# Optimization experiments

Hardware: AMD Instinct MI355X
Metric: run time of the kernel (lower is better)

The kernel has to match this reference:

```python
import jax, jax.numpy as jnp
import numpy as np

ND, NPR, DD, DP, LAT, AT, B = 2048, 2048, 128, 128, 128, 32, 16384


def setup_inputs():
    key = jax.random.key(0)
    ks = jax.random.split(key, 20)
    s = 0.05
    d = {}
    d["e_p_adj"] = (jax.random.uniform(ks[0], (ND, NPR)) < 0.05).astype(jnp.float32)
    d["e_e_adj"] = (jax.random.uniform(ks[1], (ND, ND)) < 0.05).astype(jnp.float32)
    d["p_p_adj"] = (jax.random.uniform(ks[2], (NPR, NPR)) < 0.05).astype(jnp.float32)
    d["input_disease"] = jax.random.randint(ks[3], (B,), 0, ND)
    d["input_drug"] = jax.random.randint(ks[4], (B,), 0, NPR)
    d["labels"] = jax.random.randint(ks[5], (B,), 0, 2)
    # learned parameters
    d["disease_emb"] = jax.random.normal(ks[6], (ND, DD)) * s
    d["drug_emb"] = jax.random.normal(ks[7], (NPR, DP)) * s
    d["Wdg"] = jax.random.normal(ks[8], (DP, LAT)) * s   # disease_gcn_w
    d["bdg_lin"] = jnp.zeros((LAT,))                      # Linear bias
    d["bdg"] = jnp.zeros((LAT,))                          # extra disease_gcn_b
    d["Wpg"] = jax.random.normal(ks[9], (DD, LAT)) * s   # drug_gcn_w
    d["bpg_lin"] = jnp.zeros((LAT,))
    d["bpg"] = jnp.zeros((LAT,))
    d["Wa1_d"] = jax.random.normal(ks[10], (DP + DD, AT)) * s  # concat [key(drug), query(disease)]
    d["ba1_d"] = jnp.zeros((AT,))
    d["Wa2_d"] = jax.random.normal(ks[11], (AT, 1)) * s
    d["ba2_d"] = jnp.zeros((1,))
    d["Wa1_p"] = jax.random.normal(ks[12], (DD + DP, AT)) * s  # concat [key(disease), query(drug)]
    d["ba1_p"] = jnp.zeros((AT,))
    d["Wa2_p"] = jax.random.normal(ks[13], (AT, 1)) * s
    d["ba2_p"] = jnp.zeros((1,))
    d["Wd2"] = jax.random.normal(ks[14], (DD, LAT)) * s  # disease_w2
    d["bd2"] = jnp.zeros((LAT,))
    d["Wp3"] = jax.random.normal(ks[15], (DP, LAT)) * s  # drug_w3
    d["bp3"] = jnp.zeros((LAT,))
    d["mlp_W1"] = jax.random.normal(ks[16], (LAT, DD)) * s
    d["mlp_b1"] = jnp.zeros((DD,))
    d["mlp_W2"] = jax.random.normal(ks[17], (DD, DD)) * s
    d["mlp_b2"] = jnp.zeros((DD,))
    d["Wpred"] = jax.random.normal(ks[18], (DD, 1)) * s
    d["bpred"] = jnp.zeros((1,))
    return d


def _attention_gcn(adj, other, selfe, W1, b1, W2, b2):
    # torch: concat([key=other, query=self]) -> Linear(W1) ; split W1 instead of
    # materializing the [Ns, No, Dk+Dq] concat tensor (same math, less HBM traffic)
    do = other.shape[1]
    ko = other @ W1[:do]              # [No, A]
    qs = selfe @ W1[do:]              # [Ns, A]
    h = jax.nn.relu(qs[:, None, :] + ko[None, :, :] + b1)   # [Ns, No, A]
    alpha = jax.nn.relu(jnp.squeeze(h @ W2, -1) + b2[0])    # [Ns, No]
    alpha = alpha * adj
    return jax.nn.softmax(alpha, axis=1) @ other            # [Ns, Do]


def _forward(e_p_adj, e_e_adj, p_p_adj, input_disease, input_drug, labels,
             disease_emb, drug_emb, Wdg, bdg_lin, bdg, Wpg, bpg_lin, bpg,
             Wa1_d, ba1_d, Wa2_d, ba2_d, Wa1_p, ba1_p, Wa2_p, ba2_p,
             Wd2, bd2, Wp3, bp3, mlp_W1, mlp_b1, mlp_W2, mlp_b2, Wpred, bpred):
    h_e_gcn = _attention_gcn(e_p_adj, drug_emb, disease_emb, Wa1_d, ba1_d, Wa2_d, ba2_d)
    h_e_gcn = h_e_gcn @ Wdg + bdg_lin + bdg
    h_p_gcn = _attention_gcn(e_p_adj.T, disease_emb, drug_emb, Wa1_p, ba1_p, Wa2_p, ba2_p)
    h_p_gcn = h_p_gcn @ Wpg + bpg_lin + bpg
    # disease knn branch
    deg_d = jnp.sum(e_e_adj, axis=1, keepdims=True) + 1e-8
    h_e_e = ((e_e_adj @ disease_emb) / deg_d) @ Wd2 + bd2
    h_e = jax.nn.selu(h_e_gcn + h_e_e)
    # drug knn branch
    deg_p = jnp.sum(p_p_adj, axis=1, keepdims=True) + 1e-8
    h_p_p = ((p_p_adj @ drug_emb) / deg_p) @ Wp3 + bp3
    h_p = jax.nn.selu(h_p_gcn + h_p_p)
    # pair prediction MLP
    x = h_e[input_disease] * h_p[input_drug]                # [B, LAT]
    x = jax.nn.selu(x @ mlp_W1 + mlp_b1)
    x = jax.nn.selu(x @ mlp_W2 + mlp_b2)
    z = jnp.squeeze(x @ Wpred, -1) + bpred[0]               # [B]
    y = labels.astype(jnp.float32)
    # BCEWithLogitsLoss (stable), mean reduction
    loss = jnp.mean(jnp.maximum(z, 0.0) - z * y + jnp.log1p(jnp.exp(-jnp.abs(z))))
    return (loss, jax.nn.sigmoid(z))


def reference(e_p_adj, e_e_adj, p_p_adj, input_disease, input_drug, labels,
              disease_emb, drug_emb, Wdg, bdg_lin, bdg, Wpg, bpg_lin, bpg,
              Wa1_d, ba1_d, Wa2_d, ba2_d, Wa1_p, ba1_p, Wa2_p, ba2_p,
              Wd2, bd2, Wp3, bp3, mlp_W1, mlp_b1, mlp_W2, mlp_b2, Wpred, bpred):
    return _forward(e_p_adj, e_e_adj, p_p_adj, input_disease, input_drug, labels,
                    disease_emb, drug_emb, Wdg, bdg_lin, bdg, Wpg, bpg_lin, bpg,
                    Wa1_d, ba1_d, Wa2_d, ba2_d, Wa1_p, ba1_p, Wa2_p, ba2_p,
                    Wd2, bd2, Wp3, bp3, mlp_W1, mlp_b1, mlp_W2, mlp_b2, Wpred, bpred)
```

## Files before the change

kernel.cpp:

```cpp
#include <hip/hip_runtime.h>

#define ND   2048
#define BB   16384

typedef unsigned short u16;
typedef unsigned int u32;
typedef __attribute__((ext_vector_type(8))) short short8;
typedef __attribute__((ext_vector_type(4))) float f32x4;

__device__ inline float bf2f(u16 u) {
    union { u32 i; float f; } v; v.i = ((u32)u) << 16; return v.f;
}
__device__ inline u16 f2bf(float f) {
    union { float f; u32 i; } v; v.f = f;
    u32 i = v.i + 0x7fffu + ((v.i >> 16) & 1u);
    return (u16)(i >> 16);
}
__device__ inline float seluf(float x) {
    const float sc = 1.0507009873554805f, al = 1.6732632423543772f;
    return x > 0.f ? sc * x : sc * al * expm1f(x);
}
__device__ inline short8 packbf8(float4 f0, float4 f1) {
    short8 a;
    a[0] = (short)f2bf(f0.x); a[1] = (short)f2bf(f0.y);
    a[2] = (short)f2bf(f0.z); a[3] = (short)f2bf(f0.w);
    a[4] = (short)f2bf(f1.x); a[5] = (short)f2bf(f1.y);
    a[6] = (short)f2bf(f1.z); a[7] = (short)f2bf(f1.w);
    return a;
}

__global__ void detectk(const void* __restrict__ demb, u32* __restrict__ flag) {
    const u16* p = (const u16*)demb;
    int tid = threadIdx.x;
    int sane = 0;
    #pragma unroll
    for (int i = 0; i < 2; i++) {
        u16 u = p[4 * tid + 2 * i];
        int e = (u >> 7) & 0xFF;
        if (u == 0 || (e >= 0x66 && e <= 0x8C)) sane++;
    }
    __shared__ int red[256];
    red[tid] = sane; __syncthreads();
    for (int o = 128; o > 0; o >>= 1) {
        if (tid < o) red[tid] += red[tid + o];
        __syncthreads();
    }
    if (tid == 0) flag[0] = (red[0] < 300) ? 1u : 0u;
}

#define NSEG 26
struct CvtArgs { const void* src[NSEG]; int off[NSEG]; int n[NSEG]; };

__global__ __launch_bounds__(256) void cvtk(CvtArgs a, u16* __restrict__ base,
                                            const u32* __restrict__ flag) {
    int seg = blockIdx.y;
    int n = a.n[seg];
    const void* s = a.src[seg];
    u16* d = base + a.off[seg];
    bool f32 = flag[0] != 0;
    int stride = gridDim.x * blockDim.x;
    for (int i = blockIdx.x * blockDim.x + threadIdx.x; i < n; i += stride)
        d[i] = f32 ? f2bf(((const float*)s)[i]) : ((const u16*)s)[i];
}

__device__ inline void tpose_body(const u16* in, int R, int C,
                                  u16* out, int ldo, int ooff,
                                  u16 (*tile)[33]) {
    int c0 = blockIdx.x * 32, r0 = blockIdx.y * 32;
    int x = c0 + threadIdx.x;
    for (int i = threadIdx.y; i < 32; i += 8) {
        int r = r0 + i;
        tile[i][threadIdx.x] = (r < R && x < C) ? in[(size_t)r * C + x] : (u16)0;
    }
    __syncthreads();
    int rr = r0 + threadIdx.x;
    for (int i = threadIdx.y; i < 32; i += 8) {
        int cc = c0 + i;
        if (cc < C && rr < R) out[(size_t)cc * ldo + ooff + rr] = tile[threadIdx.x][i];
    }
}

__global__ void tpose_smalls(const u16* s0, const u16* s1, const u16* s2,
                             const u16* s3, const u16* s4, const u16* s5,
                             u16* W1T, u16* W2T, u16* WcTe, u16* WcTp) {
    __shared__ u16 tile[32][33];
    const u16* in; u16* out; int ldo, ooff;
    switch (blockIdx.z) {
        case 0:  in = s0; out = W1T;  ldo = 128; ooff = 0;   break;
        case 1:  in = s1; out = W2T;  ldo = 128; ooff = 0;   break;
        case 2:  in = s2; out = WcTe; ldo = 256; ooff = 0;   break;
        case 3:  in = s3; out = WcTe; ldo = 256; ooff = 128; break;
        case 4:  in = s4; out = WcTp; ldo = 256; ooff = 0;   break;
        default: in = s5; out = WcTp; ldo = 256; ooff = 128; break;
    }
    tpose_body(in, 128, 128, out, ldo, ooff, tile);
}

__global__ __launch_bounds__(256) void colsump(const u16* __restrict__ demb,
                                               const u16* __restrict__ pemb,
                                               float* __restrict__ part) {
    int m = blockIdx.y;
    const u16* e = m ? pemb : demb;
    int t = threadIdx.x;
    int c2 = t & 63, rg = t >> 6;
    int r0 = blockIdx.x * 64;
    float s0 = 0.f, s1 = 0.f;
    for (int i = 0; i < 16; i++) {
        u32 v = *(const u32*)(e + (size_t)(r0 + i * 4 + rg) * 128 + c2 * 2);
        s0 += bf2f((u16)(v & 0xffffu));
        s1 += bf2f((u16)(v >> 16));
    }
    __shared__ float t0[256], t1[256];
    t0[t] = s0; t1[t] = s1;
    __syncthreads();
    if (t < 64) {
        float a0 = t0[t] + t0[t + 64] + t0[t + 128] + t0[t + 192];
        float a1 = t1[t] + t1[t + 64] + t1[t + 128] + t1[t + 192];
        part[(size_t)m * 4096 + blockIdx.x * 128 + t * 2 + 0] = a0;
        part[(size_t)m * 4096 + blockIdx.x * 128 + t * 2 + 1] = a1;
    }
}

__global__ void biasc(const u16* a0, const u16* a1, const u16* a2, u16* o0,
                      const u16* b0, const u16* b1, const u16* b2, u16* o1,
                      const float* __restrict__ part,
                      float* __restrict__ csd, float* __restrict__ csp) {
    int t = threadIdx.x;
    o0[t] = f2bf(bf2f(a0[t]) + bf2f(a1[t]) + bf2f(a2[t]));
    o1[t] = f2bf(bf2f(b0[t]) + bf2f(b1[t]) + bf2f(b2[t]));
    float sd = 0.f, sp = 0.f;
    for (int b = 0; b < 32; b++) {
        sd += part[b * 128 + t];
        sp += part[4096 + b * 128 + t];
    }
    csd[t] = sd;
    csp[t] = sp;
}

__global__ __launch_bounds__(128) void koqs(
    const u16* __restrict__ demb, const u16* __restrict__ pemb,
    const u16* __restrict__ Wa1d, const u16* __restrict__ ba1d,
    const u16* __restrict__ Wa1p, const u16* __restrict__ ba1p,
    float* __restrict__ ko_d, float* __restrict__ qs_d,
    float* __restrict__ ko_p, float* __restrict__ qs_p) {
    int row = blockIdx.x, m = blockIdx.y, tid = threadIdx.x;
    const u16* src; const u16* W; const u16* bias; float* out;
    switch (m) {
        case 0:  src = pemb; W = Wa1d;            bias = nullptr; out = ko_d; break;
        case 1:  src = demb; W = Wa1d + 128 * 32; bias = ba1d;    out = qs_d; break;
        case 2:  src = demb; W = Wa1p;            bias = nullptr; out = ko_p; break;
        default: src = pemb; W = Wa1p + 128 * 32; bias = ba1p;    out = qs_p; break;
    }
    __shared__ float x[128];
    __shared__ float red[128];
    x[tid] = bf2f(src[(size_t)row * 128 + tid]);
    __syncthreads();
    int a = tid & 31, part = tid >> 5;
    float s = 0.f;
    #pragma unroll
    for (int k = 0; k < 32; k++) s += x[part * 32 + k] * bf2f(W[(part * 32 + k) * 32 + a]);
    red[tid] = s;
    __syncthreads();
    if (part == 0) {
        float t = red[a] + red[a + 32] + red[a + 64] + red[a + 96];
        if (bias) t += bf2f(bias[a]);
        out[(size_t)row * 32 + a] = t;
    }
}

struct CS {
    const void* adj[3];
    u16* ridx[3]; u32* rcnt[3];
    u16* cidx; u32* ccnt;
};

__global__ __launch_bounds__(256) void csrbuild(CS c, const u32* __restrict__ flag) {
    int m = blockIdx.y, r = blockIdx.x, t = threadIdx.x;
    int lane = t & 63;
    bool f32 = flag[0] != 0;
    __shared__ u32 lcnt;
    if (t == 0) lcnt = 0;
    __syncthreads();
    float v[8];
    int c0 = t * 8;
    if (f32) {
        const float4* p = (const float4*)((const float*)c.adj[m] + (size_t)r * 2048 + c0);
        float4 x = p[0], y = p[1];
        v[0] = x.x; v[1] = x.y; v[2] = x.z; v[3] = x.w;
        v[4] = y.x; v[5] = y.y; v[6] = y.z; v[7] = y.w;
    } else {
        const uint4* p = (const uint4*)((const u16*)c.adj[m] + (size_t)r * 2048 + c0);
        uint4 x = p[0];
        u32 u[4] = {x.x, x.y, x.z, x.w};
        #pragma unroll
        for (int i = 0; i < 4; i++) {
            v[2 * i + 0] = (u[i] & 0xffffu) ? 1.f : 0.f;
            v[2 * i + 1] = (u[i] >> 16)     ? 1.f : 0.f;
        }
    }
    int cnt = 0;
    #pragma unroll
    for (int i = 0; i < 8; i++) cnt += (v[i] != 0.f) ? 1 : 0;
    int pfx = cnt;
    #pragma unroll
    for (int o = 1; o < 64; o <<= 1) {
        int s = __shfl_up(pfx, o, 64);
        if (lane >= o) pfx += s;
    }
    int wtot = __shfl(pfx, 63, 64);
    u32 wb = 0;
    if (lane == 0) wb = atomicAdd(&lcnt, (u32)wtot);
    wb = __shfl((int)wb, 0, 64);
    int o = (int)wb + pfx - cnt;
    u16* ridx = c.ridx[m] + (size_t)r * 2048;
    #pragma unroll
    for (int i = 0; i < 8; i++) {
        if (v[i] != 0.f) {
            ridx[o++] = (u16)(c0 + i);
            if (m == 0) {
                u32 q = atomicAdd(&c.ccnt[c0 + i], 1u);
                c.cidx[(size_t)(c0 + i) * 2048 + q] = (u16)r;
            }
        }
    }
    __syncthreads();
    if (t == 0) c.rcnt[m][r] = lcnt;
}

struct SP {
    const u16* idx[4]; const u32* cnt[4];
    const float* ko[4]; const float* qs[4];
    const u16* w2[4]; const u16* b2[4];
    const u16* emb[4]; const float* csum[4];
    u16* out[4]; int ooff[4]; int attn[4];
};

__global__ __launch_bounds__(256) void spagg(SP a) {
    int task = blockIdx.y;
    int tid = threadIdx.x;
    int wv = tid >> 6, lane = tid & 63;
    int grp = lane >> 4, dim = lane & 15;
    int r = blockIdx.x * 4 + wv;
    const u16* idx = a.idx[task] + (size_t)r * 2048;
    int nnz = (int)a.cnt[task][r];
    int isat = a.attn[task];
    const u16* emb = a.emb[task];
    const float* ko = a.ko[task];

    float qsr[32], w2h[32];
    float b2v = 0.f;
    if (isat) {
        const float4* qp = (const float4*)(a.qs[task] + (size_t)r * 32);
        #pragma unroll
        for (int i = 0; i < 8; i++) {
            float4 v = qp[i];
            qsr[4 * i + 0] = v.x; qsr[4 * i + 1] = v.y;
            qsr[4 * i + 2] = v.z; qsr[4 * i + 3] = v.w;
        }
        #pragma unroll
        for (int i = 0; i < 32; i++) w2h[i] = bf2f(a.w2[task][i]);
        b2v = bf2f(a.b2[task][0]);
    }

    float acc[8];
    #pragma unroll
    for (int t = 0; t < 8; t++) acc[t] = 0.f;
    float wsuml = 0.f;

    for (int base = 0; base < nnz; base += 64) {
        int i = base + lane;
        float w = 0.f;
        int j = 0;
        if (i < nnz) {
            j = (int)idx[i];
            if (isat) {
                const float4* kp = (const float4*)(ko + (size_t)j * 32);
                float s = 0.f;
                #pragma unroll
                for (int q = 0; q < 8; q++) {
                    float4 kv = kp[q];
                    s += fmaxf(qsr[4 * q + 0] + kv.x, 0.f) * w2h[4 * q + 0];
                    s += fmaxf(qsr[4 * q + 1] + kv.y, 0.f) * w2h[4 * q + 1];
                    s += fmaxf(qsr[4 * q + 2] + kv.z, 0.f) * w2h[4 * q + 2];
                    s += fmaxf(qsr[4 * q + 3] + kv.w, 0.f) * w2h[4 * q + 3];
                }
                w = __expf(fmaxf(s + b2v, 0.f)) - 1.f;
            } else {
                w = 1.f;
            }
        }
        wsuml += w;
        int cend = min(64, nnz - base);
        #pragma unroll 4
        for (int k4 = 0; k4 < cend; k4 += 4) {
            int kk = k4 + grp;
            float wk = __shfl(w, kk, 64);
            int jk = __shfl(j, kk, 64);
            const uint4* p = (const uint4*)((const char*)emb + jk * 256 + dim * 16);
            uint4 vv = *p;
            u32 u[4] = {vv.x, vv.y, vv.z, vv.w};
            #pragma unroll
            for (int cc = 0; cc < 4; cc++) {
                acc[2 * cc + 0] = fmaf(wk, bf2f((u16)(u[cc] & 0xffffu)), acc[2 * cc + 0]);
                acc[2 * cc + 1] = fmaf(wk, bf2f((u16)(u[cc] >> 16)), acc[2 * cc + 1]);
            }
        }
    }

    #pragma unroll
    for (int t = 0; t < 8; t++) {
        acc[t] += __shfl_xor(acc[t], 32, 64);
        acc[t] += __shfl_xor(acc[t], 16, 64);
    }
    #pragma unroll
    for (int o = 32; o > 0; o >>= 1) wsuml += __shfl_xor(wsuml, o, 64);

    if (grp == 0) {
        float v[8];
        if (isat) {
            float sc = 1.f / (2048.f + wsuml);
            const float* cs = a.csum[task] + dim * 8;
            #pragma unroll
            for (int t = 0; t < 8; t++) v[t] = (cs[t] + acc[t]) * sc;
        } else {
            float sc = 1.f / (wsuml + 1e-8f);
            #pragma unroll
            for (int t = 0; t < 8; t++) v[t] = acc[t] * sc;
        }
        uint4 pk;
        pk.x = (u32)f2bf(v[0]) | ((u32)f2bf(v[1]) << 16);
        pk.y = (u32)f2bf(v[2]) | ((u32)f2bf(v[3]) << 16);
        pk.z = (u32)f2bf(v[4]) | ((u32)f2bf(v[5]) << 16);
        pk.w = (u32)f2bf(v[6]) | ((u32)f2bf(v[7]) << 16);
        *(uint4*)(a.out[task] + (size_t)r * 256 + a.ooff[task] + dim * 8) = pk;
    }
}

struct GD4 {
    const void* A[4]; const u16* BT[4]; u16* C[4];
    const u16* bias[4]; const float* rs[4];
    int lda[4], ldb[4], ldc[4], coff[4], kiters[4], act[4], araw[4], rsmode[4];
};

#define PADK 136

__global__ __launch_bounds__(256, 2) void gemmL(GD4 g, const u32* __restrict__ flag) {
    __shared__ __align__(16) u16 As[16][PADK];
    __shared__ __align__(16) u16 Bs[128][PADK];
    int z = blockIdx.y;
    bool af32 = g.araw[z] && (flag[0] != 0);
    const void* A = g.A[z];
    const u16* BT = g.BT[z];
    int lda = g.lda[z], ldb = g.ldb[z];
    int kiters = g.kiters[z];
    int tid = threadIdx.x;
    int lane = tid & 63, wv = tid >> 6;
    int mrow = lane & 15, quad = lane >> 4;
    int m0 = blockIdx.x * 16;
    int c0 = wv * 32;
    int sr = tid >> 4, sk = (tid & 15) * 8;
    f32x4 acc0 = {0.f, 0.f, 0.f, 0.f}, acc1 = {0.f, 0.f, 0.f, 0.f};

    short8 ra, rb[8];
    auto ldstage = [&](int kb) {
        if (af32) {
            const float* A32 = (const float*)A;
            const float4* p = (const float4*)(A32 + (size_t)(m0 + sr) * lda + kb + sk);
            float4 f0 = p[0], f1 = p[1];
            ra = packbf8(f0, f1);
        } else {
            ra = *(const short8*)((const u16*)A + (size_t)(m0 + sr) * lda + kb + sk);
        }
        const u16* bbase = BT + (size_t)sr * ldb + kb + sk;
        #pragma unroll
        for (int i = 0; i < 8; i++)
            rb[i] = *(const short8*)(bbase + (size_t)i * 16 * ldb);
    };
    auto ststage = [&]() {
        *(short8*)(&As[sr][sk]) = ra;
        #pragma unroll
        for (int i = 0; i < 8; i++)
            *(short8*)(&Bs[i * 16 + sr][sk]) = rb[i];
    };
    auto compute = [&]() {
        #pragma unroll
        for (int ks = 0; ks < 4; ks++) {
            short8 af = *(const short8*)(&As[mrow][ks * 32 + quad * 8]);
            short8 b0 = *(const short8*)(&Bs[c0 + mrow][ks * 32 + quad * 8]);
            short8 b1 = *(const short8*)(&Bs[c0 + 16 + mrow][ks * 32 + quad * 8]);
            acc0 = __builtin_amdgcn_mfma_f32_16x16x32_bf16(af, b0, acc0, 0, 0, 0);
            acc1 = __builtin_amdgcn_mfma_f32_16x16x32_bf16(af, b1, acc1, 0, 0, 0);
        }
    };

    ldstage(0);
    #pragma unroll 1
    for (int it = 0; it < kiters - 1; ++it) {
        ststage();
        __syncthreads();
        ldstage((it + 1) * 128);
        compute();
        __syncthreads();
    }
    ststage();
    __syncthreads();
    compute();

    const float* rs = g.rs[z];
    int rsmode = g.rsmode[z];
    const u16* bi = g.bias[z];
    u16* C = g.C[z];
    int ldc = g.ldc[z], coff = g.coff[z], act = g.act[z];
    int n0 = c0 + mrow, n1 = n0 + 16;
    float bv0 = bi ? bf2f(bi[n0]) : 0.f;
    float bv1 = bi ? bf2f(bi[n1]) : 0.f;
    #pragma unroll
    for (int r = 0; r < 4; r++) {
        int row = m0 + quad * 4 + r;
        float v0 = acc0[r], v1 = acc1[r];
        if (rsmode == 1) { float sc = rs[row]; v0 *= sc; v1 *= sc; }
        else if (rsmode == 2) {
            float t = 0.f;
            #pragma unroll
            for (int p = 0; p < 8; p++) t += rs[row + p * 2048];
            float sc = 1.f / t;
            v0 *= sc; v1 *= sc;
        }
        v0 += bv0; v1 += bv1;
        if (act) { v0 = seluf(v0); v1 = seluf(v1); }
        C[(size_t)row * ldc + coff + n0] = f2bf(v0);
        C[(size_t)row * ldc + coff + n1] = f2bf(v1);
    }
}

__global__ __launch_bounds__(256) void xbuild(
    const u16* __restrict__ he, const u16* __restrict__ hp,
    const int* __restrict__ di, const int* __restrict__ dr, u16* __restrict__ X) {
    int idx = blockIdx.x * 256 + threadIdx.x;
    int d2 = idx & 63;
    int b = idx >> 6;
    int ia = di[b], ic = dr[b];
    u32 ue = ((const u32*)he)[ia * 64 + d2];
    u32 up = ((const u32*)hp)[ic * 64 + d2];
    float lo = bf2f((u16)(ue & 0xffff)) * bf2f((u16)(up & 0xffff));
    float hi = bf2f((u16)(ue >> 16)) * bf2f((u16)(up >> 16));
    ((u32*)X)[idx] = (u32)f2bf(lo) | ((u32)f2bf(hi) << 16);
}

__global__ __launch_bounds__(256) void zloss(
    const u16* __restrict__ X2, const u16* __restrict__ wpred,
    const u16* __restrict__ bpred, const int* __restrict__ labels,
    float* __restrict__ out, float* __restrict__ part) {
    __shared__ float wp[128];
    __shared__ float ls[256];
    int tid = threadIdx.x;
    if (tid < 128) wp[tid] = bf2f(wpred[tid]);
    __syncthreads();
    int b = blockIdx.x * 256 + tid;
    const uint4* xp = (const uint4*)(X2 + (size_t)b * 128);
    float z = 0.f;
    #pragma unroll
    for (int i = 0; i < 16; i++) {
        uint4 q = xp[i];
        u32 u[4] = {q.x, q.y, q.z, q.w};
        #pragma unroll
        for (int c = 0; c < 4; c++) {
            z += bf2f((u16)(u[c] & 0xffff)) * wp[i * 8 + c * 2];
            z += bf2f((u16)(u[c] >> 16)) * wp[i * 8 + c * 2 + 1];
        }
    }
    z += bf2f(bpred[0]);
    out[1 + b] = 1.f / (1.f + __expf(-z));
    float y = (float)labels[b];
    ls[tid] = fmaxf(z, 0.f) - z * y + log1pf(__expf(-fabsf(z)));
    __syncthreads();
    for (int o = 128; o > 0; o >>= 1) {
        if (tid < o) ls[tid] += ls[tid + o];
        __syncthreads();
    }
    if (tid == 0) part[blockIdx.x] = ls[0];
}

__global__ void finloss(const float* __restrict__ part, float* __restrict__ out) {
    __shared__ float s[64];
    s[threadIdx.x] = part[threadIdx.x];
    __syncthreads();
    for (int o = 32; o > 0; o >>= 1) {
        if (threadIdx.x < o) s[threadIdx.x] += s[threadIdx.x + o];
        __syncthreads();
    }
    if (threadIdx.x == 0) out[0] = s[0] * (1.f / 16384.f);
}

extern "C" void kernel_launch(void* const* d_in, const int* in_sizes, int n_in,
                              void* d_out, int out_size, void* d_ws, size_t ws_size,
                              hipStream_t stream) {
    const void* e_p_adj = d_in[0];
    const void* e_e_adj = d_in[1];
    const void* p_p_adj = d_in[2];
    const int* in_dis  = (const int*)d_in[3];
    const int* in_drug = (const int*)d_in[4];
    const int* labels  = (const int*)d_in[5];
    float* out = (float*)d_out;

    char* ws = (char*)d_ws;
    size_t off = 0;
    auto take = [&](size_t bytes) { char* p = ws + off; off = (off + bytes + 255) & ~(size_t)255; return p; };
    u16*   A_e   = (u16*)take((size_t)2048 * 256 * 2);
    u16*   A_p   = (u16*)take((size_t)2048 * 256 * 2);
    u16*   WcTe  = (u16*)take((size_t)128 * 256 * 2);
    u16*   WcTp  = (u16*)take((size_t)128 * 256 * 2);
    u16*   W1T   = (u16*)take((size_t)128 * 128 * 2);
    u16*   W2T   = (u16*)take((size_t)128 * 128 * 2);
    u16*   b_e   = (u16*)take(256);
    u16*   b_p   = (u16*)take(256);
    u16*   h_e   = (u16*)take((size_t)2048 * 128 * 2);
    u16*   h_p   = (u16*)take((size_t)2048 * 128 * 2);
    float* ko_d  = (float*)take((size_t)2048 * 32 * 4);
    float* qs_d  = (float*)take((size_t)2048 * 32 * 4);
    float* ko_p  = (float*)take((size_t)2048 * 32 * 4);
    float* qs_p  = (float*)take((size_t)2048 * 32 * 4);
    float* cspart = (float*)take((size_t)2 * 32 * 128 * 4);
    float* csd   = (float*)take(128 * 4);
    float* csp   = (float*)take(128 * 4);
    float* part  = (float*)take(64 * 4);
    u32*   flag  = (u32*)take(256);
    u16*   canon = (u16*)take((size_t)700000 * 2);
    u16*   X     = (u16*)take((size_t)BB * 128 * 2);
    u16*   X1    = (u16*)take((size_t)BB * 128 * 2);
    u16*   X2    = (u16*)take((size_t)BB * 128 * 2);
    u16*   idx0  = (u16*)take((size_t)2048 * 2048 * 2);
    u16*   idx1  = (u16*)take((size_t)2048 * 2048 * 2);
    u16*   idx2  = (u16*)take((size_t)2048 * 2048 * 2);
    u16*   idx3  = (u16*)take((size_t)2048 * 2048 * 2);
    u32*   cnt0  = (u32*)take(2048 * 4);
    u32*   cnt2  = (u32*)take(2048 * 4);
    u32*   cnt3  = (u32*)take(2048 * 4);
    u32*   cntT  = (u32*)take(2048 * 4);

    const int segidx[NSEG] = {6, 7, 14, 18, 8, 22, 11, 24, 26, 28,
                              15, 16, 17, 19, 20, 21,
                              9, 10, 12, 13, 23, 25, 27, 29, 30, 31};
    const int segn[NSEG]   = {262144, 262144, 8192, 8192, 16384, 16384, 16384, 16384, 16384, 16384,
                              32, 32, 1, 32, 32, 1,
                              128, 128, 128, 128, 128, 128, 128, 128, 128, 1};
    CvtArgs ca;
    u16* cp[NSEG];
    {
        int o = 0;
        for (int i = 0; i < NSEG; i++) {
            ca.src[i] = d_in[segidx[i]];
            ca.off[i] = o;
            ca.n[i] = segn[i];
            cp[i] = canon + o;
            o += (segn[i] + 15) & ~15;
        }
    }
    u16 *cdemb = cp[0], *cpemb = cp[1], *cWa1d = cp[2], *cWa1p = cp[3];
    u16 *cWdg = cp[4], *cWd2 = cp[5], *cWpg = cp[6], *cWp3 = cp[7];
    u16 *cW1 = cp[8], *cW2 = cp[9];
    u16 *cba1d = cp[10], *cWa2d = cp[11], *cba2d = cp[12];
    u16 *cba1p = cp[13], *cWa2p = cp[14], *cba2p = cp[15];
    u16 *cbdg_lin = cp[16], *cbdg = cp[17], *cbpg_lin = cp[18], *cbpg = cp[19];
    u16 *cbd2 = cp[20], *cbp3 = cp[21], *cmb1 = cp[22], *cmb2 = cp[23];
    u16 *cWpred = cp[24], *cbpred = cp[25];

    detectk<<<1, 256, 0, stream>>>(d_in[6], flag);
    cvtk<<<dim3(64, NSEG), 256, 0, stream>>>(ca, canon, flag);

    hipMemsetAsync(cntT, 0, 2048 * sizeof(u32), stream);
    {
        CS cs;
        cs.adj[0] = e_p_adj; cs.ridx[0] = idx0; cs.rcnt[0] = cnt0;
        cs.adj[1] = e_e_adj; cs.ridx[1] = idx2; cs.rcnt[1] = cnt2;
        cs.adj[2] = p_p_adj; cs.ridx[2] = idx3; cs.rcnt[2] = cnt3;
        cs.cidx = idx1; cs.ccnt = cntT;
        csrbuild<<<dim3(2048, 3), 256, 0, stream>>>(cs, flag);
    }

    colsump<<<dim3(32, 2), 256, 0, stream>>>(cdemb, cpemb, cspart);
    tpose_smalls<<<dim3(4, 4, 6), dim3(32, 8), 0, stream>>>(
        cW1, cW2, cWdg, cWd2, cWpg, cWp3, W1T, W2T, WcTe, WcTp);
    biasc<<<1, 128, 0, stream>>>(cbdg_lin, cbdg, cbd2, b_e, cbpg_lin, cbpg, cbp3, b_p,
                                 cspart, csd, csp);
    koqs<<<dim3(2048, 4), 128, 0, stream>>>(cdemb, cpemb, cWa1d, cba1d, cWa1p, cba1p,
                                            ko_d, qs_d, ko_p, qs_p);

    {
        SP sp;
        sp.idx[0] = idx0; sp.cnt[0] = cnt0; sp.ko[0] = ko_d; sp.qs[0] = qs_d;
        sp.w2[0] = cWa2d; sp.b2[0] = cba2d; sp.emb[0] = cpemb; sp.csum[0] = csp;
        sp.out[0] = A_e; sp.ooff[0] = 0; sp.attn[0] = 1;
        sp.idx[1] = idx2; sp.cnt[1] = cnt2; sp.ko[1] = ko_d; sp.qs[1] = qs_d;
        sp.w2[1] = cWa2d; sp.b2[1] = cba2d; sp.emb[1] = cdemb; sp.csum[1] = csd;
        sp.out[1] = A_e; sp.ooff[1] = 128; sp.attn[1] = 0;
        sp.idx[2] = idx1; sp.cnt[2] = cntT; sp.ko[2] = ko_p; sp.qs[2] = qs_p;
        sp.w2[2] = cWa2p; sp.b2[2] = cba2p; sp.emb[2] = cdemb; sp.csum[2] = csd;
        sp.out[2] = A_p; sp.ooff[2] = 0; sp.attn[2] = 1;
        sp.idx[3] = idx3; sp.cnt[3] = cnt3; sp.ko[3] = ko_p; sp.qs[3] = qs_p;
        sp.w2[3] = cWa2p; sp.b2[3] = cba2p; sp.emb[3] = cpemb; sp.csum[3] = csp;
        sp.out[3] = A_p; sp.ooff[3] = 128; sp.attn[3] = 0;
        spagg<<<dim3(512, 4), 256, 0, stream>>>(sp);
    }

    auto setd = [](GD4& g, int z, const void* A, int lda, const u16* BT, int ldb,
                   u16* C, int ldc, int coff, int ki, const u16* bi,
                   const float* rs, int act, int araw, int rm) {
        g.A[z] = A; g.lda[z] = lda; g.BT[z] = BT; g.ldb[z] = ldb;
        g.C[z] = C; g.ldc[z] = ldc; g.coff[z] = coff; g.kiters[z] = ki;
        g.bias[z] = bi; g.rs[z] = rs; g.act[z] = act; g.araw[z] = araw; g.rsmode[z] = rm;
    };

    {
        GD4 g;
        setd(g, 0, A_e, 256, WcTe, 256, h_e, 128, 0, 2, b_e, nullptr, 1, 0, 0);
        setd(g, 1, A_p, 256, WcTp, 256, h_p, 128, 0, 2, b_p, nullptr, 1, 0, 0);
        setd(g, 2, A_e, 256, WcTe, 256, h_e, 128, 0, 2, b_e, nullptr, 1, 0, 0);
        setd(g, 3, A_e, 256, WcTe, 256, h_e, 128, 0, 2, b_e, nullptr, 1, 0, 0);
        gemmL<<<dim3(128, 2), 256, 0, stream>>>(g, flag);
    }

    xbuild<<<4096, 256, 0, stream>>>(h_e, h_p, in_dis, in_drug, X);
    {
        GD4 g;
        setd(g, 0, X, 128, W1T, 128, X1, 128, 0, 1, cmb1, nullptr, 1, 0, 0);
        setd(g, 1, X, 128, W1T, 128, X1, 128, 0, 1, cmb1, nullptr, 1, 0, 0);
        setd(g, 2, X, 128, W1T, 128, X1, 128, 0, 1, cmb1, nullptr, 1, 0, 0);
        setd(g, 3, X, 128, W1T, 128, X1, 128, 0, 1, cmb1, nullptr, 1, 0, 0);
        gemmL<<<dim3(1024, 1), 256, 0, stream>>>(g, flag);
    }
    {
        GD4 g;
        setd(g, 0, X1, 128, W2T, 128, X2, 128, 0, 1, cmb2, nullptr, 1, 0, 0);
        setd(g, 1, X1, 128, W2T, 128, X2, 128, 0, 1, cmb2, nullptr, 1, 0, 0);
        setd(g, 2, X1, 128, W2T, 128, X2, 128, 0, 1, cmb2, nullptr, 1, 0, 0);
        setd(g, 3, X1, 128, W2T, 128, X2, 128, 0, 1, cmb2, nullptr, 1, 0, 0);
        gemmL<<<dim3(1024, 1), 256, 0, stream>>>(g, flag);
    }

    zloss<<<64, 256, 0, stream>>>(X2, cWpred, cbpred, labels, out, part);
    finloss<<<1, 64, 0, stream>>>(part, out);
}
```

Before: 254.0 us.

## Fuse pair-gather MLP and loss into one kernel; split transpose CSR build

Replaces the separate gather, two MLP GEMM launches and the loss kernel with one fused kernel. Each block gathers 64 pair rows into shared memory, runs both 128x128 layers with MFMA, and reduces the prediction dot product and loss partials in registers. This removes the three 16384x128 intermediate buffers and their global round-trips. It also moves the transposed-CSR atomics out of the dense adjacency scan into a separate kernel that walks the compact row index, and drops the now-unused fp32 A-path in gemmL. Costs include an extra kernel launch and only 256 blocks for the fused MLP.

```diff
diff --git a/kernel.cpp b/kernel.cpp
--- a/kernel.cpp
+++ b/kernel.cpp
@@ -19,14 +19,6 @@
 __device__ inline float seluf(float x) {
     const float sc = 1.0507009873554805f, al = 1.6732632423543772f;
     return x > 0.f ? sc * x : sc * al * expm1f(x);
-}
-__device__ inline short8 packbf8(float4 f0, float4 f1) {
-    short8 a;
-    a[0] = (short)f2bf(f0.x); a[1] = (short)f2bf(f0.y);
-    a[2] = (short)f2bf(f0.z); a[3] = (short)f2bf(f0.w);
-    a[4] = (short)f2bf(f1.x); a[5] = (short)f2bf(f1.y);
-    a[6] = (short)f2bf(f1.z); a[7] = (short)f2bf(f1.w);
-    return a;
 }
 
 __global__ void detectk(const void* __restrict__ demb, u32* __restrict__ flag) {
@@ -171,7 +163,6 @@
 struct CS {
     const void* adj[3];
     u16* ridx[3]; u32* rcnt[3];
-    u16* cidx; u32* ccnt;
 };
 
 __global__ __launch_bounds__(256) void csrbuild(CS c, const u32* __restrict__ flag) {
@@ -215,16 +206,24 @@
     u16* ridx = c.ridx[m] + (size_t)r * 2048;
     #pragma unroll
     for (int i = 0; i < 8; i++) {
-        if (v[i] != 0.f) {
-            ridx[o++] = (u16)(c0 + i);
-            if (m == 0) {
-                u32 q = atomicAdd(&c.ccnt[c0 + i], 1u);
-                c.cidx[(size_t)(c0 + i) * 2048 + q] = (u16)r;
-            }
-        }
+        if (v[i] != 0.f) ridx[o++] = (u16)(c0 + i);
     }
     __syncthreads();
     if (t == 0) c.rcnt[m][r] = lcnt;
+}
+
+__global__ __launch_bounds__(128) void colbuild(const u16* __restrict__ idx0,
+                                                const u32* __restrict__ cnt0,
+                                                u16* __restrict__ cidx,
+                                                u32* __restrict__ ccnt) {
+    int r = blockIdx.x;
+    int n = (int)cnt0[r];
+    const u16* row = idx0 + (size_t)r * 2048;
+    for (int i = threadIdx.x; i < n; i += 128) {
+        int c = (int)row[i];
+        u32 q = atomicAdd(&ccnt[c], 1u);
+        cidx[(size_t)c * 2048 + q] = (u16)r;
+    }
 }
 
 struct SP {
@@ -348,7 +347,6 @@
     __shared__ __align__(16) u16 As[16][PADK];
     __shared__ __align__(16) u16 Bs[128][PADK];
     int z = blockIdx.y;
-    bool af32 = g.araw[z] && (flag[0] != 0);
     const void* A = g.A[z];
     const u16* BT = g.BT[z];
     int lda = g.lda[z], ldb = g.ldb[z];
@@ -363,14 +361,7 @@
 
     short8 ra, rb[8];
     auto ldstage = [&](int kb) {
-        if (af32) {
-            const float* A32 = (const float*)A;
-            const float4* p = (const float4*)(A32 + (size_t)(m0 + sr) * lda + kb + sk);
-            float4 f0 = p[0], f1 = p[1];
-            ra = packbf8(f0, f1);
-        } else {
-            ra = *(const short8*)((const u16*)A + (size_t)(m0 + sr) * lda + kb + sk);
-        }
+        ra = *(const short8*)((const u16*)A + (size_t)(m0 + sr) * lda + kb + sk);
         const u16* bbase = BT + (size_t)sr * ldb + kb + sk;
         #pragma unroll
         for (int i = 0; i < 8; i++)
@@ -433,63 +424,141 @@
     }
 }
 
-__global__ __launch_bounds__(256) void xbuild(
+#define PADX 136
+__global__ __launch_bounds__(256, 2) void mlpfused(
     const u16* __restrict__ he, const u16* __restrict__ hp,
-    const int* __restrict__ di, const int* __restrict__ dr, u16* __restrict__ X) {
-    int idx = blockIdx.x * 256 + threadIdx.x;
-    int d2 = idx & 63;
-    int b = idx >> 6;
-    int ia = di[b], ic = dr[b];
-    u32 ue = ((const u32*)he)[ia * 64 + d2];
-    u32 up = ((const u32*)hp)[ic * 64 + d2];
-    float lo = bf2f((u16)(ue & 0xffff)) * bf2f((u16)(up & 0xffff));
-    float hi = bf2f((u16)(ue >> 16)) * bf2f((u16)(up >> 16));
-    ((u32*)X)[idx] = (u32)f2bf(lo) | ((u32)f2bf(hi) << 16);
-}
-
-__global__ __launch_bounds__(256) void zloss(
-    const u16* __restrict__ X2, const u16* __restrict__ wpred,
-    const u16* __restrict__ bpred, const int* __restrict__ labels,
+    const int* __restrict__ di, const int* __restrict__ dr,
+    const u16* __restrict__ W1T, const u16* __restrict__ b1,
+    const u16* __restrict__ W2T, const u16* __restrict__ b2,
+    const u16* __restrict__ wpred, const u16* __restrict__ bpred,
+    const int* __restrict__ labels,
     float* __restrict__ out, float* __restrict__ part) {
-    __shared__ float wp[128];
-    __shared__ float ls[256];
+    __shared__ __align__(16) u16 Xs[64][PADX];
+    __shared__ __align__(16) u16 Ws[128][PADX];
+    __shared__ float wred[4];
     int tid = threadIdx.x;
-    if (tid < 128) wp[tid] = bf2f(wpred[tid]);
-    __syncthreads();
-    int b = blockIdx.x * 256 + tid;
-    const uint4* xp = (const uint4*)(X2 + (size_t)b * 128);
-    float z = 0.f;
-    #pragma unroll
-    for (int i = 0; i < 16; i++) {
-        uint4 q = xp[i];
-        u32 u[4] = {q.x, q.y, q.z, q.w};
-        #pragma unroll
-        for (int c = 0; c < 4; c++) {
-            z += bf2f((u16)(u[c] & 0xffff)) * wp[i * 8 + c * 2];
-            z += bf2f((u16)(u[c] >> 16)) * wp[i * 8 + c * 2 + 1];
-        }
-    }
-    z += bf2f(bpred[0]);
-    out[1 + b] = 1.f / (1.f + __expf(-z));
-    float y = (float)labels[b];
-    ls[tid] = fmaxf(z, 0.f) - z * y + log1pf(__expf(-fabsf(z)));
+    int lane = tid & 63, wv = tid >> 6;
+    int mrow = lane & 15, quad = lane >> 4;
+    int p0 = blockIdx.x * 64;
+
+    {
+        int row = tid >> 2, sub = tid & 3;
+        int b = p0 + row;
+        int ia = di[b], ic = dr[b];
+        const uint4* pe = (const uint4*)(he + (size_t)ia * 128 + sub * 32);
+        const uint4* pp = (const uint4*)(hp + (size_t)ic * 128 + sub * 32);
+        #pragma unroll
+        for (int q = 0; q < 4; q++) {
+            uint4 ue = pe[q], up = pp[q];
+            u32 eu[4] = {ue.x, ue.y, ue.z, ue.w};
+            u32 pu[4] = {up.x, up.y, up.z, up.w};
+            #pragma unroll
+            for (int c = 0; c < 4; c++) {
+                float lo = bf2f((u16)(eu[c] & 0xffffu)) * bf2f((u16)(pu[c] & 0xffffu));
+                float hi = bf2f((u16)(eu[c] >> 16)) * bf2f((u16)(pu[c] >> 16));
+                *(u32*)(&Xs[row][sub * 32 + q * 8 + c * 2]) =
+                    (u32)f2bf(lo) | ((u32)f2bf(hi) << 16);
+            }
+        }
+    }
+    {
+        int n = tid >> 1, half = tid & 1;
+        const short8* src = (const short8*)(W1T + (size_t)n * 128 + half * 64);
+        short8* dst = (short8*)(&Ws[n][half * 64]);
+        #pragma unroll
+        for (int i = 0; i < 8; i++) dst[i] = src[i];
+    }
+    __syncthreads();
+
+    f32x4 acc[8];
+    #pragma unroll
+    for (int nt = 0; nt < 8; nt++) acc[nt] = {0.f, 0.f, 0.f, 0.f};
+    #pragma unroll
+    for (int ks = 0; ks < 4; ks++) {
+        short8 af = *(const short8*)(&Xs[wv * 16 + mrow][ks * 32 + quad * 8]);
+        #pragma unroll
+        for (int nt = 0; nt < 8; nt++) {
+            short8 bfv = *(const short8*)(&Ws[nt * 16 + mrow][ks * 32 + quad * 8]);
+            acc[nt] = __builtin_amdgcn_mfma_f32_16x16x32_bf16(af, bfv, acc[nt], 0, 0, 0);
+        }
+    }
+    __syncthreads();
+    #pragma unroll
+    for (int nt = 0; nt < 8; nt++) {
+        int col = nt * 16 + mrow;
+        float bv = bf2f(b1[col]);
+        #pragma unroll
+        for (int r = 0; r < 4; r++) {
+            int row = wv * 16 + quad * 4 + r;
+            Xs[row][col] = f2bf(seluf(acc[nt][r] + bv));
+        }
+    }
+    {
+        int n = tid >> 1, half = tid & 1;
+        const short8* src = (const short8*)(W2T + (size_t)n * 128 + half * 64);
+        short8* dst = (short8*)(&Ws[n][half * 64]);
+        #pragma unroll
+        for (int i = 0; i < 8; i++) dst[i] = src[i];
+    }
+    __syncthreads();
+
+    #pragma unroll
+    for (int nt = 0; nt < 8; nt++) acc[nt] = {0.f, 0.f, 0.f, 0.f};
+    #pragma unroll
+    for (int ks = 0; ks < 4; ks++) {
+        short8 af = *(const short8*)(&Xs[wv * 16 + mrow][ks * 32 + quad * 8]);
+        #pragma unroll
+        for (int nt = 0; nt < 8; nt++) {
+            short8 bfv = *(const short8*)(&Ws[nt * 16 + mrow][ks * 32 + quad * 8]);
+            acc[nt] = __builtin_amdgcn_mfma_f32_16x16x32_bf16(af, bfv, acc[nt], 0, 0, 0);
+        }
+    }
+
+    float zp[4] = {0.f, 0.f, 0.f, 0.f};
+    #pragma unroll
+    for (int nt = 0; nt < 8; nt++) {
+        int col = nt * 16 + mrow;
+        float bv = bf2f(b2[col]);
+        float wp = bf2f(wpred[col]);
+        #pragma unroll
+        for (int r = 0; r < 4; r++) {
+            float x2 = bf2f(f2bf(seluf(acc[nt][r] + bv)));
+            zp[r] = fmaf(x2, wp, zp[r]);
+        }
+    }
+    #pragma unroll
+    for (int r = 0; r < 4; r++) {
+        #pragma unroll
+        for (int o = 1; o < 16; o <<= 1) zp[r] += __shfl_xor(zp[r], o, 64);
+    }
+    float bpv = bf2f(bpred[0]);
+    float lsum = 0.f;
+    #pragma unroll
+    for (int r = 0; r < 4; r++) {
+        int b = p0 + wv * 16 + quad * 4 + r;
+        float z = zp[r] + bpv;
+        float sig = 1.f / (1.f + __expf(-z));
+        if (mrow == 0) out[1 + b] = sig;
+        float y = (float)labels[b];
+        lsum += fmaxf(z, 0.f) - z * y + log1pf(__expf(-fabsf(z)));
+    }
+    lsum += __shfl_xor(lsum, 16, 64);
+    lsum += __shfl_xor(lsum, 32, 64);
+    if (lane == 0) wred[wv] = lsum;
+    __syncthreads();
+    if (tid == 0) part[blockIdx.x] = wred[0] + wred[1] + wred[2] + wred[3];
+}
+
+__global__ void finloss(const float* __restrict__ part, float* __restrict__ out) {
+    __shared__ float s[256];
+    int t = threadIdx.x;
+    s[t] = part[t];
     __syncthreads();
     for (int o = 128; o > 0; o >>= 1) {
-        if (tid < o) ls[tid] += ls[tid + o];
+        if (t < o) s[t] += s[t + o];
         __syncthreads();
     }
-    if (tid == 0) part[blockIdx.x] = ls[0];
-}
-
-__global__ void finloss(const float* __restrict__ part, float* __restrict__ out) {
-    __shared__ float s[64];
-    s[threadIdx.x] = part[threadIdx.x];
-    __syncthreads();
-    for (int o = 32; o > 0; o >>= 1) {
-        if (threadIdx.x < o) s[threadIdx.x] += s[threadIdx.x + o];
-        __syncthreads();
-    }
-    if (threadIdx.x == 0) out[0] = s[0] * (1.f / 16384.f);
+    if (t == 0) out[0] = s[0] * (1.f / 16384.f);
 }
 
 extern "C" void kernel_launch(void* const* d_in, const int* in_sizes, int n_in,
@@ -523,12 +592,9 @@
     float* cspart = (float*)take((size_t)2 * 32 * 128 * 4);
     float* csd   = (float*)take(128 * 4);
     float* csp   = (float*)take(128 * 4);
-    float* part  = (float*)take(64 * 4);
+    float* part  = (float*)take(256 * 4);
     u32*   flag  = (u32*)take(256);
     u16*   canon = (u16*)take((size_t)700000 * 2);
-    u16*   X     = (u16*)take((size_t)BB * 128 * 2);
-    u16*   X1    = (u16*)take((size_t)BB * 128 * 2);
-    u16*   X2    = (u16*)take((size_t)BB * 128 * 2);
     u16*   idx0  = (u16*)take((size_t)2048 * 2048 * 2);
     u16*   idx1  = (u16*)take((size_t)2048 * 2048 * 2);
     u16*   idx2  = (u16*)take((size_t)2048 * 2048 * 2);
@@ -574,9 +640,9 @@
         cs.adj[0] = e_p_adj; cs.ridx[0] = idx0; cs.rcnt[0] = cnt0;
         cs.adj[1] = e_e_adj; cs.ridx[1] = idx2; cs.rcnt[1] = cnt2;
         cs.adj[2] = p_p_adj; cs.ridx[2] = idx3; cs.rcnt[2] = cnt3;
-        cs.cidx = idx1; cs.ccnt = cntT;
         csrbuild<<<dim3(2048, 3), 256, 0, stream>>>(cs, flag);
     }
+    colbuild<<<2048, 128, 0, stream>>>(idx0, cnt0, idx1, cntT);
 
     colsump<<<dim3(32, 2), 256, 0, stream>>>(cdemb, cpemb, cspart);
     tpose_smalls<<<dim3(4, 4, 6), dim3(32, 8), 0, stream>>>(
@@ -620,24 +686,8 @@
         gemmL<<<dim3(128, 2), 256, 0, stream>>>(g, flag);
     }
 
-    xbuild<<<4096, 256, 0, stream>>>(h_e, h_p, in_dis, in_drug, X);
-    {
-        GD4 g;
-        setd(g, 0, X, 128, W1T, 128, X1, 128, 0, 1, cmb1, nullptr, 1, 0, 0);
-        setd(g, 1, X, 128, W1T, 128, X1, 128, 0, 1, cmb1, nullptr, 1, 0, 0);
-        setd(g, 2, X, 128, W1T, 128, X1, 128, 0, 1, cmb1, nullptr, 1, 0, 0);
-        setd(g, 3, X, 128, W1T, 128, X1, 128, 0, 1, cmb1, nullptr, 1, 0, 0);
-        gemmL<<<dim3(1024, 1), 256, 0, stream>>>(g, flag);
-    }
-    {
-        GD4 g;
-        setd(g, 0, X1, 128, W2T, 128, X2, 128, 0, 1, cmb2, nullptr, 1, 0, 0);
-        setd(g, 1, X1, 128, W2T, 128, X2, 128, 0, 1, cmb2, nullptr, 1, 0, 0);
-        setd(g, 2, X1, 128, W2T, 128, X2, 128, 0, 1, cmb2, nullptr, 1, 0, 0);
-        setd(g, 3, X1, 128, W2T, 128, X2, 128, 0, 1, cmb2, nullptr, 1, 0, 0);
-        gemmL<<<dim3(1024, 1), 256, 0, stream>>>(g, flag);
-    }
-
-    zloss<<<64, 256, 0, stream>>>(X2, cWpred, cbpred, labels, out, part);
-    finloss<<<1, 64, 0, stream>>>(part, out);
-}
+    mlpfused<<<256, 256, 0, stream>>>(h_e, h_p, in_dis, in_drug,
+                                      W1T, cmb1, W2T, cmb2,
+                                      cWpred, cbpred, labels, out, part);
+    finloss<<<1, 256, 0, stream>>>(part, out);
+}
```

Measured after the change: 242.6 us. 4.5% less time.
